# Kernel optimization log

Measured on AMD Instinct MI355X. Metric: run time of the kernel, lower is better.

Reference implementation:

```python
import jax, jax.numpy as jnp
import numpy as np

B, T, C, HS = 8, 4096, 1024, 128

def setup_inputs() -> dict:
    key = jax.random.key(0)
    kx, kq, kk, kv = jax.random.split(key, 4)
    x = jax.random.normal(kx, (B, T, C), dtype=jnp.float32)
    # Linear weights stored as [in, out] so projection is x @ W
    Wq = jax.random.normal(kq, (C, HS), dtype=jnp.float32) * (C ** -0.5)
    Wk = jax.random.normal(kk, (C, HS), dtype=jnp.float32) * (C ** -0.5)
    Wv = jax.random.normal(kv, (C, HS), dtype=jnp.float32) * (C ** -0.5)
    return {"x": x, "Wq": Wq, "Wk": Wk, "Wv": Wv}

def reference(x, Wq, Wk, Wv):
    # one head of causal self-attention (dropout=0.0 -> identity)
    q = x @ Wq  # [B,T,HS]
    k = x @ Wk
    v = x @ Wv
    scale = q.shape[-1] ** -0.5
    scores = jnp.einsum('bqd,bkd->bqk', q, k) * scale  # [B,T,T]
    t = q.shape[1]
    causal = jnp.tril(jnp.ones((t, t), dtype=bool))
    scores = jnp.where(causal, scores, jnp.finfo(scores.dtype).min)
    weights = jax.nn.softmax(scores, axis=-1)
    out = jnp.einsum('bqk,bkd->bqd', weights, v)  # [B,T,HS]
    return out
```

## Files before the change

kernel.cpp:

```cpp
#include <hip/hip_runtime.h>
#include <hip/hip_bf16.h>

#define TB 8
#define TT 4096
#define TC 1024
#define THS 128

typedef __bf16 bf16;
typedef __attribute__((ext_vector_type(8))) __bf16 bf16x8;
typedef __attribute__((ext_vector_type(2))) __bf16 bf16x2;
typedef __attribute__((ext_vector_type(4))) float f32x4;
typedef __attribute__((ext_vector_type(16))) float f32x16;

__device__ __forceinline__ unsigned pkbf(float a, float b) {
    bf16x2 t = { (bf16)a, (bf16)b };
    return __builtin_bit_cast(unsigned, t);
}

__device__ __forceinline__ void gload16(const void* g, void* l) {
    __builtin_amdgcn_global_load_lds(
        (const __attribute__((address_space(1))) void*)g,
        (__attribute__((address_space(3))) void*)l, 16, 0, 0);
}

__global__ __launch_bounds__(256) void wt_kernel(const float* __restrict__ Wq,
                                                 const float* __restrict__ Wk,
                                                 const float* __restrict__ Wv,
                                                 bf16* __restrict__ Wt) {
    __shared__ float tile[64][65];
    const int tid = threadIdx.x;
    const int idx = blockIdx.x;
    const int w = idx >> 5;
    const int kt = (idx & 31) >> 1, ntb = idx & 1;
    const int k0 = kt * 64, n0 = ntb * 64;
    const float* W = (w == 0) ? Wq : (w == 1) ? Wk : Wv;
    #pragma unroll
    for (int i = 0; i < 4; i++) {
        int r = (tid >> 4) + i * 16;
        int c4 = (tid & 15) * 4;
        float4 x4 = *reinterpret_cast<const float4*>(&W[(long)(k0 + r) * 128 + n0 + c4]);
        tile[r][c4 + 0] = x4.x; tile[r][c4 + 1] = x4.y;
        tile[r][c4 + 2] = x4.z; tile[r][c4 + 3] = x4.w;
    }
    __syncthreads();
    const int n = tid >> 2, kk = (tid & 3) * 16;
    bf16 o[16];
    #pragma unroll
    for (int j = 0; j < 16; j++) o[j] = (bf16)tile[kk + j][n];
    bf16* dst = &Wt[(long)((w << 7) + n0 + n) * 1024 + k0 + kk];
    *reinterpret_cast<bf16x8*>(dst)     = *reinterpret_cast<bf16x8*>(&o[0]);
    *reinterpret_cast<bf16x8*>(dst + 8) = *reinterpret_cast<bf16x8*>(&o[8]);
}

__global__ __launch_bounds__(512, 4) void qkv_kernel(const float* __restrict__ x,
                                                     const bf16* __restrict__ Wt,
                                                     bf16* __restrict__ Q,
                                                     bf16* __restrict__ K,
                                                     bf16* __restrict__ Vtt) {
    __shared__ __align__(1024) char smem[81920];
    const int tid = threadIdx.x;
    const int wave = tid >> 6, lane = tid & 63;
    const int lr = lane & 15, g = lane >> 4;
    const int qs = wave >> 2, ns = wave & 3;
    const long row0 = (long)blockIdx.x * 64;

    int xOff[2], xL[2];
    #pragma unroll
    for (int i = 0; i < 2; i++) {
        int D = wave * 2048 + i * 1024 + lane * 16;
        int r = D >> 8, c = D & 255;
        xOff[i] = r * 4096 + (c ^ (((r & 7) << 4) ^ (((r >> 3) & 1) << 7)));
        xL[i] = wave * 2048 + i * 1024;
    }
    int wOff[6], wL[6];
    #pragma unroll
    for (int i = 0; i < 6; i++) {
        int D = wave * 6144 + i * 1024 + lane * 16;
        int n = D >> 7, c = D & 127;
        wOff[i] = n * 2048 + (c ^ ((n & 7) << 4));
        wL[i] = wave * 6144 + i * 1024;
    }
    const char* xb = (const char*)x + row0 * 4096;
    const char* wb = (const char*)Wt;

    f32x4 acc[2][6] = {};

    {
        #pragma unroll
        for (int i = 0; i < 2; i++) gload16(xb + xOff[i], smem + xL[i]);
        #pragma unroll
        for (int i = 0; i < 6; i++) gload16(wb + wOff[i], smem + 32768 + wL[i]);
        #pragma unroll
        for (int i = 0; i < 2; i++) gload16(xb + 256 + xOff[i], smem + 16384 + xL[i]);
    }

    #pragma unroll 1
    for (int s = 0; s < 16; s++) {
        if (s < 15) asm volatile("s_waitcnt vmcnt(2)" ::: "memory");
        else        asm volatile("s_waitcnt vmcnt(0)" ::: "memory");
        __builtin_amdgcn_s_barrier();

        const char* xp = smem + (s & 1) * 16384;
        const char* wp = smem + 32768;
        bf16x8 a[2][2];
        #pragma unroll
        for (int ar = 0; ar < 2; ar++) {
            const int r = qs * 32 + ar * 16 + lr;
            const int rs = ((r & 7) << 4) ^ (((r >> 3) & 1) << 7);
            #pragma unroll
            for (int ks = 0; ks < 2; ks++) {
                f32x4 lo  = *reinterpret_cast<const f32x4*>(xp + r * 256 + ((ks * 128 + g * 32) ^ rs));
                f32x4 hi4 = *reinterpret_cast<const f32x4*>(xp + r * 256 + ((ks * 128 + g * 32 + 16) ^ rs));
                uint4 u;
                u.x = pkbf(lo[0], lo[1]);  u.y = pkbf(lo[2], lo[3]);
                u.z = pkbf(hi4[0], hi4[1]); u.w = pkbf(hi4[2], hi4[3]);
                a[ar][ks] = __builtin_bit_cast(bf16x8, u);
            }
        }
        __builtin_amdgcn_s_setprio(1);
        #pragma unroll
        for (int nt = 0; nt < 6; nt++) {
            const int n = ns * 96 + nt * 16 + lr;
            const int nsw = (n & 7) << 4;
            #pragma unroll
            for (int ks = 0; ks < 2; ks++) {
                bf16x8 bfr = *reinterpret_cast<const bf16x8*>(wp + n * 128 + ((ks * 64 + g * 16) ^ nsw));
                #pragma unroll
                for (int ar = 0; ar < 2; ar++)
                    acc[ar][nt] = __builtin_amdgcn_mfma_f32_16x16x32_bf16(a[ar][ks], bfr, acc[ar][nt], 0, 0, 0);
            }
        }
        __builtin_amdgcn_s_setprio(0);
        __builtin_amdgcn_s_barrier();

        if (s + 1 < 16) {
            #pragma unroll
            for (int i = 0; i < 6; i++)
                gload16(wb + (s + 1) * 128 + wOff[i], smem + 32768 + wL[i]);
        }
        if (s + 2 < 16) {
            #pragma unroll
            for (int i = 0; i < 2; i++)
                gload16(xb + (s + 2) * 256 + xOff[i], smem + (s & 1) * 16384 + xL[i]);
        }
    }

    const float qscale = 0.08838834764831845f;
    bf16* ld = (bf16*)smem;
    #pragma unroll 1
    for (int wsel = 0; wsel < 3; wsel++) {
        __syncthreads();
        #pragma unroll
        for (int nt = 0; nt < 6; nt++) {
            const int colbase = ns * 96 + nt * 16;
            if ((colbase >> 7) != wsel) continue;
            const int d = (colbase + lr) & 127;
            #pragma unroll
            for (int ar = 0; ar < 2; ar++)
                #pragma unroll
                for (int r = 0; r < 4; r++) {
                    float val = acc[ar][nt][r];
                    if (wsel == 0) val *= qscale;
                    const int lrow = qs * 32 + ar * 16 + g * 4 + r;
                    ld[lrow * 136 + d] = (bf16)val;
                }
        }
        __syncthreads();
        if (wsel < 2) {
            bf16* dst = (wsel == 0 ? Q : K) + row0 * 128;
            #pragma unroll
            for (int i = 0; i < 2; i++) {
                const int slot = tid + 512 * i;
                const int rr = slot >> 4, c8 = (slot & 15) * 8;
                bf16x8 vv = *reinterpret_cast<const bf16x8*>(&ld[rr * 136 + c8]);
                *reinterpret_cast<bf16x8*>(&dst[rr * 128 + c8]) = vv;
            }
        } else {
            bf16* dst = Vtt + (long)blockIdx.x * 8192;
            #pragma unroll
            for (int i = 0; i < 2; i++) {
                const int slot = tid + 512 * i;
                const int d = slot >> 3, t8 = (slot & 7) * 8;
                bf16x8 vv;
                #pragma unroll
                for (int j = 0; j < 8; j++) vv[j] = ld[(t8 + j) * 136 + d];
                *reinterpret_cast<bf16x8*>(&dst[d * 64 + t8]) = vv;
            }
        }
    }
}

__global__ __launch_bounds__(512, 2) void attn_kernel(const bf16* __restrict__ Q,
                                                      const bf16* __restrict__ K,
                                                      const bf16* __restrict__ Vtt,
                                                      float* __restrict__ out) {
    __shared__ __align__(1024) char smem[131072];
    __shared__ float mlb[6 * 64];
    const int tid = threadIdx.x;
    const int wave = tid >> 6, lane = tid & 63;
    const int c = lane & 31, hi = lane >> 5;
    const int qs = wave >> 2, kvq = wave & 3;
    const int kswz = ((c & 7) << 4) ^ (((c >> 3) & 1) << 7);
    const int vswz = (c & 7) << 4;
    const int v = blockIdx.x >> 3, b = blockIdx.x & 7;
    const long base = (long)b * TT * 128;
    const char* Kb = (const char*)(K + base);
    const char* Vb = (const char*)Vtt + (long)b * (64 * 16384);

    int kOff[4], vOff[4], lOff[4];
    #pragma unroll
    for (int i = 0; i < 4; i++) {
        int D = wave * 4096 + i * 1024 + lane * 16;
        kOff[i] = (D & ~255) | ((D & 255) ^ (((D >> 8) & 7) << 4) ^ (((D >> 11) & 1) << 7));
        vOff[i] = (D & ~127) | ((D & 127) ^ (((D >> 7) & 7) << 4));
        lOff[i] = wave * 4096 + i * 1024;
    }

    #pragma unroll 1
    for (int ph = 0; ph < 2; ph++) {
        const int qt = ph ? 63 - v : v;
        const int nIt = (qt + 2) >> 1;
        const int q0w = qt * 64 + qs * 32;
        const int qa = q0w + c;

        bf16x8 qf[8];
        #pragma unroll
        for (int dw = 0; dw < 8; dw++)
            qf[dw] = *reinterpret_cast<const bf16x8*>(&Q[base + (long)qa * 128 + dw * 16 + hi * 8]);

        f32x16 O[4] = {};
        float m = -__builtin_inff(), l = 0.f;

        {
            #pragma unroll
            for (int i = 0; i < 4; i++) {
                gload16(Kb + kOff[i], smem + lOff[i]);
                gload16(Vb + vOff[i], smem + 65536 + lOff[i]);
            }
            if (nIt > 1) {
                #pragma unroll
                for (int i = 0; i < 4; i++) {
                    gload16(Kb + 32768 + kOff[i], smem + 32768 + lOff[i]);
                    gload16(Vb + 32768 + vOff[i], smem + 98304 + lOff[i]);
                }
            }
        }

        #pragma unroll 1
        for (int it = 0; it < nIt; it++) {
            const int bi = it & 1;
            char* kBuf = smem + bi * 32768;
            char* vBuf = smem + 65536 + bi * 32768;
            if (it + 1 < nIt) asm volatile("s_waitcnt vmcnt(8)" ::: "memory");
            else              asm volatile("s_waitcnt vmcnt(0)" ::: "memory");
            __builtin_amdgcn_s_barrier();

            const int kv0 = it * 128 + kvq * 32;
            if (kv0 <= q0w) {
                const char* kb = kBuf + kvq * 8192;
                const char* vb = vBuf + (kvq >> 1) * 16384;
                const int vcol0 = (kvq & 1) * 64;
                f32x16 S = {};
                __builtin_amdgcn_s_setprio(1);
                #pragma unroll
                for (int dw = 0; dw < 8; dw++) {
                    bf16x8 kf = *reinterpret_cast<const bf16x8*>(
                        kb + c * 256 + ((dw * 32 + hi * 16) ^ kswz));
                    S = __builtin_amdgcn_mfma_f32_32x32x16_bf16(kf, qf[dw], S, 0, 0, 0);
                }
                __builtin_amdgcn_s_setprio(0);
                if (kv0 == q0w) {
                    #pragma unroll
                    for (int i = 0; i < 16; i++) {
                        int kvr = kv0 + (i & 3) + 8 * (i >> 2) + 4 * hi;
                        if (kvr > qa) S[i] = -__builtin_inff();
                    }
                }
                float t8[8];
                #pragma unroll
                for (int i = 0; i < 8; i++) t8[i] = fmaxf(S[i], S[i + 8]);
                float t4a = fmaxf(t8[0], t8[4]), t4b = fmaxf(t8[1], t8[5]);
                float t4c = fmaxf(t8[2], t8[6]), t4d = fmaxf(t8[3], t8[7]);
                float pm = fmaxf(fmaxf(t4a, t4b), fmaxf(t4c, t4d));
                pm = fmaxf(pm, __shfl_xor(pm, 32, 64));
                if (!__all(pm - m <= 8.0f)) {
                    float mn = fmaxf(m, pm);
                    float fr = __expf(m - mn);
                    #pragma unroll
                    for (int dt = 0; dt < 4; dt++) O[dt] = O[dt] * fr;
                    l *= fr;
                    m = mn;
                }
                #pragma unroll
                for (int i = 0; i < 16; i++) S[i] = __expf(S[i] - m);
                float s8[8];
                #pragma unroll
                for (int i = 0; i < 8; i++) s8[i] = S[i] + S[i + 8];
                l += ((s8[0] + s8[4]) + (s8[1] + s8[5])) + ((s8[2] + s8[6]) + (s8[3] + s8[7]));

                bf16x8 pf[2];
                #pragma unroll
                for (int wl = 0; wl < 2; wl++) {
                    const int i0 = 8 * wl;
                    unsigned L0 = pkbf(S[i0 + 0], S[i0 + 1]);
                    unsigned L1 = pkbf(S[i0 + 2], S[i0 + 3]);
                    unsigned H0 = pkbf(S[i0 + 4], S[i0 + 5]);
                    unsigned H1 = pkbf(S[i0 + 6], S[i0 + 7]);
                    unsigned sel0 = hi ? L0 : H0;
                    unsigned sel1 = hi ? L1 : H1;
                    unsigned x0 = __shfl_xor((int)sel0, 32, 64);
                    unsigned x1 = __shfl_xor((int)sel1, 32, 64);
                    uint4 f;
                    f.x = hi ? x0 : L0;
                    f.y = hi ? x1 : L1;
                    f.z = hi ? H0 : x0;
                    f.w = hi ? H1 : x1;
                    pf[wl] = __builtin_bit_cast(bf16x8, f);
                }
                __builtin_amdgcn_s_setprio(1);
                #pragma unroll
                for (int wl = 0; wl < 2; wl++)
                    #pragma unroll
                    for (int dt = 0; dt < 4; dt++) {
                        bf16x8 vf = *reinterpret_cast<const bf16x8*>(
                            vb + (dt * 32 + c) * 128 + ((vcol0 + wl * 32 + hi * 16) ^ vswz));
                        O[dt] = __builtin_amdgcn_mfma_f32_32x32x16_bf16(vf, pf[wl], O[dt], 0, 0, 0);
                    }
                __builtin_amdgcn_s_setprio(0);
            }
            __builtin_amdgcn_s_barrier();
            if (it + 2 < nIt) {
                const char* Ks = Kb + (long)(it + 2) * 32768;
                const char* Vs = Vb + (long)(it + 2) * 32768;
                #pragma unroll
                for (int i = 0; i < 4; i++) {
                    gload16(Ks + kOff[i], kBuf + lOff[i]);
                    gload16(Vs + vOff[i], vBuf + lOff[i]);
                }
            }
        }

        l += __shfl_xor(l, 32, 64);

        if (kvq != 0) {
            const int sl = qs * 3 + (kvq - 1);
            char* om = smem + sl * 16384;
            #pragma unroll
            for (int dt = 0; dt < 4; dt++)
                #pragma unroll
                for (int g = 0; g < 4; g++) {
                    float4 w4 = { O[dt][4 * g + 0], O[dt][4 * g + 1],
                                  O[dt][4 * g + 2], O[dt][4 * g + 3] };
                    *reinterpret_cast<float4*>(
                        om + c * 512 + ((dt * 128 + g * 32 + hi * 16) ^ ((c & 7) << 4))) = w4;
                }
            if (hi == 0) { mlb[sl * 64 + c] = m; mlb[sl * 64 + 32 + c] = l; }
        }
        __syncthreads();
        if (kvq == 0) {
            float mq[3], lq[3];
            float mx = m;
            #pragma unroll
            for (int p = 0; p < 3; p++) {
                const int sl = qs * 3 + p;
                mq[p] = mlb[sl * 64 + c];
                lq[p] = mlb[sl * 64 + 32 + c];
                mx = fmaxf(mx, mq[p]);
            }
            float f0 = __expf(m - mx);
            float lt = l * f0;
            float fq[3];
            #pragma unroll
            for (int p = 0; p < 3; p++) { fq[p] = __expf(mq[p] - mx); lt += lq[p] * fq[p]; }
            float linv = 1.0f / lt;
            #pragma unroll
            for (int dt = 0; dt < 4; dt++)
                #pragma unroll
                for (int g = 0; g < 4; g++) {
                    float4 r;
                    r.x = O[dt][4 * g + 0] * f0;
                    r.y = O[dt][4 * g + 1] * f0;
                    r.z = O[dt][4 * g + 2] * f0;
                    r.w = O[dt][4 * g + 3] * f0;
                    #pragma unroll
                    for (int p = 0; p < 3; p++) {
                        const char* om = smem + (qs * 3 + p) * 16384;
                        float4 o1 = *reinterpret_cast<const float4*>(
                            om + c * 512 + ((dt * 128 + g * 32 + hi * 16) ^ ((c & 7) << 4)));
                        r.x += o1.x * fq[p]; r.y += o1.y * fq[p];
                        r.z += o1.z * fq[p]; r.w += o1.w * fq[p];
                    }
                    r.x *= linv; r.y *= linv; r.z *= linv; r.w *= linv;
                    *reinterpret_cast<float4*>(
                        &out[base + (long)qa * 128 + dt * 32 + 8 * g + 4 * hi]) = r;
                }
        }
        __syncthreads();
    }
}

extern "C" void kernel_launch(void* const* d_in, const int* in_sizes, int n_in,
                              void* d_out, int out_size, void* d_ws, size_t ws_size,
                              hipStream_t stream) {
    const float* x  = (const float*)d_in[0];
    const float* Wq = (const float*)d_in[1];
    const float* Wk = (const float*)d_in[2];
    const float* Wv = (const float*)d_in[3];
    float* out = (float*)d_out;
    bf16* Q   = (bf16*)d_ws;
    bf16* K   = Q   + (size_t)32768 * 128;
    bf16* Vtt = K   + (size_t)32768 * 128;
    bf16* Wt  = Vtt + (size_t)8 * 64 * 128 * 64;
    wt_kernel<<<96, 256, 0, stream>>>(Wq, Wk, Wv, Wt);
    qkv_kernel<<<512, 512, 0, stream>>>(x, Wt, Q, K, Vtt);
    attn_kernel<<<256, 512, 0, stream>>>(Q, K, Vtt, out);
}
```

Baseline: 114.1 us.

## Triple-buffer K and double-buffer V to drop the per-iteration trailing barrier

```diff
diff --git a/kernel.cpp b/kernel.cpp
--- a/kernel.cpp
+++ b/kernel.cpp
@@ -194,8 +194,7 @@
                                                       const bf16* __restrict__ K,
                                                       const bf16* __restrict__ Vtt,
                                                       float* __restrict__ out) {
-    __shared__ __align__(1024) char smem[131072];
-    __shared__ float mlb[6 * 64];
+    __shared__ __align__(1024) char smem[163840];
     const int tid = threadIdx.x;
     const int wave = tid >> 6, lane = tid & 63;
     const int c = lane & 31, hi = lane >> 5;
@@ -233,32 +232,38 @@
 
         {
             #pragma unroll
-            for (int i = 0; i < 4; i++) {
-                gload16(Kb + kOff[i], smem + lOff[i]);
-                gload16(Vb + vOff[i], smem + 65536 + lOff[i]);
-            }
+            for (int i = 0; i < 4; i++) gload16(Kb + kOff[i], smem + lOff[i]);
+            #pragma unroll
+            for (int i = 0; i < 4; i++) gload16(Vb + vOff[i], smem + 98304 + lOff[i]);
             if (nIt > 1) {
                 #pragma unroll
-                for (int i = 0; i < 4; i++) {
-                    gload16(Kb + 32768 + kOff[i], smem + 32768 + lOff[i]);
-                    gload16(Vb + 32768 + vOff[i], smem + 98304 + lOff[i]);
-                }
+                for (int i = 0; i < 4; i++) gload16(Kb + 32768 + kOff[i], smem + 32768 + lOff[i]);
             }
         }
 
         #pragma unroll 1
         for (int it = 0; it < nIt; it++) {
-            const int bi = it & 1;
-            char* kBuf = smem + bi * 32768;
-            char* vBuf = smem + 65536 + bi * 32768;
-            if (it + 1 < nIt) asm volatile("s_waitcnt vmcnt(8)" ::: "memory");
+            if (it + 1 < nIt) asm volatile("s_waitcnt vmcnt(4)" ::: "memory");
             else              asm volatile("s_waitcnt vmcnt(0)" ::: "memory");
             __builtin_amdgcn_s_barrier();
 
+            if (it + 1 < nIt) {
+                const char* Vs = Vb + (long)(it + 1) * 32768;
+                char* vd = smem + 98304 + ((it + 1) & 1) * 32768;
+                #pragma unroll
+                for (int i = 0; i < 4; i++) gload16(Vs + vOff[i], vd + lOff[i]);
+            }
+            if (it + 2 < nIt) {
+                const char* Ks = Kb + (long)(it + 2) * 32768;
+                char* kd = smem + ((it + 2) % 3) * 32768;
+                #pragma unroll
+                for (int i = 0; i < 4; i++) gload16(Ks + kOff[i], kd + lOff[i]);
+            }
+
             const int kv0 = it * 128 + kvq * 32;
             if (kv0 <= q0w) {
-                const char* kb = kBuf + kvq * 8192;
-                const char* vb = vBuf + (kvq >> 1) * 16384;
+                const char* kb = smem + (it % 3) * 32768 + kvq * 8192;
+                const char* vb = smem + 98304 + (it & 1) * 32768 + (kvq >> 1) * 16384;
                 const int vcol0 = (kvq & 1) * 64;
                 f32x16 S = {};
                 __builtin_amdgcn_s_setprio(1);
@@ -328,20 +333,12 @@
                     }
                 __builtin_amdgcn_s_setprio(0);
             }
-            __builtin_amdgcn_s_barrier();
-            if (it + 2 < nIt) {
-                const char* Ks = Kb + (long)(it + 2) * 32768;
-                const char* Vs = Vb + (long)(it + 2) * 32768;
-                #pragma unroll
-                for (int i = 0; i < 4; i++) {
-                    gload16(Ks + kOff[i], kBuf + lOff[i]);
-                    gload16(Vs + vOff[i], vBuf + lOff[i]);
-                }
-            }
         }
 
         l += __shfl_xor(l, 32, 64);
 
+        __syncthreads();
+        float* mlb = (float*)(smem + 161792);
         if (kvq != 0) {
             const int sl = qs * 3 + (kvq - 1);
             char* om = smem + sl * 16384;
@@ -354,7 +351,8 @@
                     *reinterpret_cast<float4*>(
                         om + c * 512 + ((dt * 128 + g * 32 + hi * 16) ^ ((c & 7) << 4))) = w4;
                 }
-            if (hi == 0) { mlb[sl * 64 + c] = m; mlb[sl * 64 + 32 + c] = l; }
+            if (hi == 0) { mlb[(qs * 3 + kvq - 1) * 64 + c] = m;
+                           mlb[(qs * 3 + kvq - 1) * 64 + 32 + c] = l; }
         }
         __syncthreads();
         if (kvq == 0) {
@@ -362,9 +360,8 @@
             float mx = m;
             #pragma unroll
             for (int p = 0; p < 3; p++) {
-                const int sl = qs * 3 + p;
-                mq[p] = mlb[sl * 64 + c];
-                lq[p] = mlb[sl * 64 + 32 + c];
+                mq[p] = mlb[(qs * 3 + p) * 64 + c];
+                lq[p] = mlb[(qs * 3 + p) * 64 + 32 + c];
                 mx = fmaxf(mx, mq[p]);
             }
             float f0 = __expf(m - mx);
```

Measured after the change: 116.6 us. 2.2% more time.
